# Optimization experiments

Hardware: AMD Instinct MI355X
Metric: run time of the kernel (lower is better)

The kernel has to match this reference:

```python
import jax, jax.numpy as jnp
import numpy as np
from jax import lax

POOL = 2  # pool_kernel

def _conv2d(x, w, b, stride=1):
    # x: [N,C,H,W], w: [O,I,kh,kw] (torch OIHW layout)
    y = lax.conv_general_dilated(
        x, w, window_strides=(stride, stride), padding='VALID',
        dimension_numbers=('NCHW', 'OIHW', 'NCHW'))
    return y + b[None, :, None, None]

def _maxpool(x, k):
    return lax.reduce_window(x, -jnp.inf, lax.max,
                             (1, 1, k, k), (1, 1, k, k), 'VALID')

def setup_inputs() -> dict:
    key = jax.random.key(0)
    ks = jax.random.split(key, 8)
    B, S, D = 8, 64, 128
    C = 32  # num_channels, depth=3 -> channels 1->32->64->64
    def kaiming(k, shape):
        fan_in = shape[1] * shape[2] * shape[3]
        return jax.random.normal(k, shape, jnp.float32) * np.float32(np.sqrt(2.0 / fan_in))
    return {
        'token_features': jax.random.normal(ks[0], (B, S, D), jnp.float32),
        'type_embedds': jax.random.normal(ks[1], (B, S, D), jnp.float32),
        'w0': kaiming(ks[2], (C, 1, 3, 3)),
        'b0': jnp.zeros((C,), jnp.float32),
        'w1': kaiming(ks[3], (2 * C, C, 3, 3)),
        'b1': jnp.zeros((2 * C,), jnp.float32),
        'w2': kaiming(ks[4], (2 * C, 2 * C, 3, 3)),
        'b2': jnp.zeros((2 * C,), jnp.float32),
    }

def reference(token_features, type_embedds, w0, b0, w1, b1, w2, b2):
    B, S, D = type_embedds.shape
    # Outter2dFusion: ger(gate, features) -> fused[b,s,i,j] = type[b,s,i]*token[b,s,j]
    fused = jnp.einsum('bsi,bsj->bsij', type_embedds, token_features)
    x = fused.reshape(B * S, 1, D, D)  # each token's d x d map as 1-channel image
    gelu = lambda t: jax.nn.gelu(t, approximate=False)  # torch GELU default (erf)
    x = _maxpool(gelu(_conv2d(x, w0, b0, stride=1)), POOL)
    x = _maxpool(gelu(_conv2d(x, w1, b1, stride=1)), POOL)
    x = _maxpool(gelu(_conv2d(x, w2, b2, stride=1)), POOL)
    # dropout is identity at inference
    return x.reshape(B, S, -1)
```

## Files before the change

### kernel.cpp

```cpp
#include <hip/hip_runtime.h>


typedef short short8 __attribute__((ext_vector_type(8)));
typedef float f32x4 __attribute__((ext_vector_type(4)));

#define OFF_TY   0
#define OFF_TK   512
#define OFF_HLO  1024
#define OFF_HHI  (1024 + 16128)
#define OFF_P0   (17152 + 8064)
#define OFF_P1   (25216 + 16896)
#define LDS_TOTAL (42112 + 1472*16)

__device__ __forceinline__ unsigned short f2bf(float f) {
    unsigned int u = __float_as_uint(f);
    u += 0x7fffu + ((u >> 16) & 1u);
    return (unsigned short)(u >> 16);
}

__device__ __forceinline__ float gelu_f(float x) {
    float ax = __builtin_fabsf(x);
    float E  = __builtin_amdgcn_exp2f(x * x * -0.72134752f);
    float k  = __builtin_amdgcn_rcpf(__builtin_fmaf(0.33267686f, ax, 1.0f));
    float s  = __builtin_fmaf(0.7478556f, k, -0.0958798f);
    s = __builtin_fmaf(s, k, 0.3480242f);
    s = s * k;
    float erfabs = __builtin_fmaf(-s, E, 1.0f);
    return __builtin_fmaf(0.5f * ax, erfabs, 0.5f * x);
}

__device__ __forceinline__ void produce(char* smem, const float* tys,
                                        float b0r, int c, int tid, int R0) {
    float t0 = tys[2*R0+0], t1 = tys[2*R0+1], t2 = tys[2*R0+2],
          t3 = tys[2*R0+3], t4 = tys[2*R0+4], t5 = tys[2*R0+5];
    int rest = tid >> 5;
    #pragma unroll
    for (int k = 0; k < 8; ++k, rest += 16) {
        if (rest < 126) {
            int roff = (rest >= 63) ? 1 : 0;
            int q = rest - (roff ? 63 : 0);
            float s0 = roff ? t2 : t0;
            float s1 = roff ? t3 : t1;
            float s2 = roff ? t4 : t2;
            float s3 = roff ? t5 : t3;
            uint2 lo = *(const uint2*)(smem + OFF_HLO + (c*126 + 2*q)*4);
            unsigned int hi = *(const unsigned int*)(smem + OFF_HHI + (c*126 + 2*q)*2);
            float h00 = __uint_as_float(lo.x << 16);
            float h10 = __uint_as_float(lo.x & 0xffff0000u);
            float h01 = __uint_as_float(lo.y << 16);
            float h11 = __uint_as_float(lo.y & 0xffff0000u);
            float h20 = __uint_as_float(hi << 16);
            float h21 = __uint_as_float(hi & 0xffff0000u);
            float e00 = __builtin_fmaf(s0,h00, __builtin_fmaf(s1,h10, __builtin_fmaf(s2,h20, b0r)));
            float e10 = __builtin_fmaf(s1,h00, __builtin_fmaf(s2,h10, __builtin_fmaf(s3,h20, b0r)));
            float e01 = __builtin_fmaf(s0,h01, __builtin_fmaf(s1,h11, __builtin_fmaf(s2,h21, b0r)));
            float e11 = __builtin_fmaf(s1,h01, __builtin_fmaf(s2,h11, __builtin_fmaf(s3,h21, b0r)));
            float m = gelu_f(fmaxf(fmaxf(e00, e01), fmaxf(e10, e11)));
            int slot = (R0 + roff) & 3;
            int unit = slot*264 + (q>>1)*8 + ((4*(q&1) + (c>>3)) ^ ((q>>1)&7));
            *(unsigned short*)(smem + OFF_P0 + unit*16 + (c&7)*2) = f2bf(m);
        }
    }
}

__launch_bounds__(512, 2)
__global__ void conv_pipeline(const float* __restrict__ token,
                              const float* __restrict__ type_,
                              const float* __restrict__ w0, const float* __restrict__ b0,
                              const float* __restrict__ w1, const float* __restrict__ b1,
                              const float* __restrict__ w2, const float* __restrict__ b2,
                              float* __restrict__ out) {
    extern __shared__ char smem[];
    float* tys = (float*)(smem + OFF_TY);
    float* tks = (float*)(smem + OFF_TK);

    const int tid = threadIdx.x;
    const int img = blockIdx.x;
    const int w   = tid >> 6;
    const int l   = tid & 63;
    const int l15 = l & 15;
    const int lc  = l >> 4;
    const int c0w = tid & 31;

    for (int i = tid; i < 128; i += 512) {
        tys[i] = type_[img*128 + i];
        tks[i] = token[img*128 + i];
    }

    const float b0r = b0[c0w];

    __syncthreads();

    {
        float w0r[9];
        #pragma unroll
        for (int i = 0; i < 9; ++i) w0r[i] = w0[c0w*9 + i];
        int x = tid >> 5;
        #pragma unroll
        for (int k = 0; k < 8; ++k, x += 16) {
            if (x < 126) {
                float t0 = tks[x], t1 = tks[x+1], t2 = tks[x+2];
                float h0 = __builtin_fmaf(w0r[0],t0, __builtin_fmaf(w0r[1],t1, w0r[2]*t2));
                float h1 = __builtin_fmaf(w0r[3],t0, __builtin_fmaf(w0r[4],t1, w0r[5]*t2));
                float h2 = __builtin_fmaf(w0r[6],t0, __builtin_fmaf(w0r[7],t1, w0r[8]*t2));
                unsigned int lov = (unsigned int)f2bf(h0) | ((unsigned int)f2bf(h1) << 16);
                *(unsigned int*)(smem + OFF_HLO + (c0w*126 + x)*4) = lov;
                *(unsigned short*)(smem + OFF_HHI + (c0w*126 + x)*2) = f2bf(h2);
            }
        }
    }

    short8 wf[18];
    float bias;
    const int ch = ((w & 3) * 16) + l15;
    if (w < 4) {
        bias = b1[ch];
        #pragma unroll
        for (int uv = 0; uv < 9; ++uv) {
            short8 f;
            #pragma unroll
            for (int j = 0; j < 8; ++j)
                f[j] = (short)f2bf(w1[(ch*32 + 8*lc + j)*9 + uv]);
            wf[uv] = f;
        }
    } else {
        bias = b2[ch];
        #pragma unroll
        for (int kh = 0; kh < 2; ++kh)
            #pragma unroll
            for (int uv = 0; uv < 9; ++uv) {
                short8 f;
                #pragma unroll
                for (int j = 0; j < 8; ++j)
                    f[j] = (short)f2bf(w2[(ch*64 + kh*32 + 8*lc + j)*9 + uv]);
                wf[kh*9 + uv] = f;
            }
    }

    __syncthreads();

    produce(smem, tys, b0r, c0w, tid, 0);
    produce(smem, tys, b0r, c0w, tid, 2);

    const size_t obase = (size_t)img * 12544;

    for (int i1 = 0; i1 < 30; ++i1) {
        __syncthreads();

        if (w < 4) {
            int rbase = (i1 % 6) * 30;
            int xr = ch >> 3;
            #pragma unroll
            for (int half = 0; half < 2; ++half) {
                f32x4 acc[4];
                #pragma unroll
                for (int i = 0; i < 4; ++i) acc[i] = (f32x4){0.f,0.f,0.f,0.f};
                #pragma unroll
                for (int pr = 0; pr < 4; ++pr) {
                    int sbase = ((2*i1 + pr) & 3) * 264;
                    #pragma unroll
                    for (int v = 0; v < 3; ++v) {
                        #pragma unroll
                        for (int mtl = 0; mtl < 2; ++mtl) {
                            int col = (2*half + mtl)*16 + l15 + v;
                            int unit = sbase + (col>>1)*8 + ((4*(col&1) + lc) ^ ((col>>1)&7));
                            short8 a = *(const short8*)(smem + OFF_P0 + unit*16);
                            if (pr <= 2)
                                acc[mtl*2+0] = __builtin_amdgcn_mfma_f32_16x16x32_bf16(
                                    a, wf[pr*3+v], acc[mtl*2+0], 0, 0, 0);
                            if (pr >= 1)
                                acc[mtl*2+1] = __builtin_amdgcn_mfma_f32_16x16x32_bf16(
                                    a, wf[(pr-1)*3+v], acc[mtl*2+1], 0, 0, 0);
                        }
                    }
                }
                #pragma unroll
                for (int mtl = 0; mtl < 2; ++mtl) {
                    int pcol = (2*half + mtl)*8 + lc*2;
                    if (pcol < 30) {
                        f32x4 A0 = acc[mtl*2+0], A1 = acc[mtl*2+1];
                        float p0 = fmaxf(fmaxf(A0[0], A0[1]), fmaxf(A1[0], A1[1]));
                        float p1 = fmaxf(fmaxf(A0[2], A0[3]), fmaxf(A1[2], A1[3]));
                        float m0 = gelu_f(p0 + bias);
                        float m1 = gelu_f(p1 + bias);
                        int u0 = (rbase + pcol)*8     + (xr ^ (pcol & 7));
                        int u1 = (rbase + pcol + 1)*8 + (xr ^ ((pcol+1) & 7));
                        *(unsigned short*)(smem + OFF_P1 + u0*16 + (ch&7)*2) = f2bf(m0);
                        *(unsigned short*)(smem + OFF_P1 + u1*16 + (ch&7)*2) = f2bf(m1);
                    }
                }
            }
        } else if (i1 >= 4 && (i1 & 1) == 0) {
            const int i2 = (i1 - 4) >> 1;
            f32x4 acc[4];
            #pragma unroll
            for (int i = 0; i < 4; ++i) acc[i] = (f32x4){0.f,0.f,0.f,0.f};
            #pragma unroll
            for (int pr = 0; pr < 4; ++pr) {
                int rb = ((2*i2 + pr) % 6) * 30;
                #pragma unroll
                for (int v = 0; v < 3; ++v) {
                    #pragma unroll
                    for (int mt = 0; mt < 2; ++mt) {
                        int col = mt*16 + l15 + v;
                        #pragma unroll
                        for (int kh = 0; kh < 2; ++kh) {
                            int unit = (rb + col)*8 + ((kh*4 + lc) ^ (col & 7));
                            short8 a = *(const short8*)(smem + OFF_P1 + unit*16);
                            if (pr <= 2)
                                acc[mt*2+0] = __builtin_amdgcn_mfma_f32_16x16x32_bf16(
                                    a, wf[kh*9 + pr*3+v], acc[mt*2+0], 0, 0, 0);
                            if (pr >= 1)
                                acc[mt*2+1] = __builtin_amdgcn_mfma_f32_16x16x32_bf16(
                                    a, wf[kh*9 + (pr-1)*3+v], acc[mt*2+1], 0, 0, 0);
                        }
                    }
                }
            }
            #pragma unroll
            for (int mt = 0; mt < 2; ++mt) {
                int pcol = mt*8 + lc*2;
                if (pcol < 14) {
                    f32x4 A0 = acc[mt*2+0], A1 = acc[mt*2+1];
                    float g00 = gelu_f(A0[0] + bias), g01 = gelu_f(A0[1] + bias);
                    float g02 = gelu_f(A0[2] + bias), g03 = gelu_f(A0[3] + bias);
                    float g10 = gelu_f(A1[0] + bias), g11 = gelu_f(A1[1] + bias);
                    float g12 = gelu_f(A1[2] + bias), g13 = gelu_f(A1[3] + bias);
                    float m0 = fmaxf(fmaxf(g00, g01), fmaxf(g10, g11));
                    float m1 = fmaxf(fmaxf(g02, g03), fmaxf(g12, g13));
                    float2 st; st.x = m0; st.y = m1;
                    *(float2*)(out + obase + ch*196 + i2*14 + pcol) = st;
                }
            }
        }

        __syncthreads();
        if (i1 < 29) produce(smem, tys, b0r, c0w, tid, 2*i1 + 4);
    }

    __syncthreads();
    if (w >= 4) {
        const int i2 = 13;
        f32x4 acc[4];
        #pragma unroll
        for (int i = 0; i < 4; ++i) acc[i] = (f32x4){0.f,0.f,0.f,0.f};
        #pragma unroll
        for (int pr = 0; pr < 4; ++pr) {
            int rb = ((2*i2 + pr) % 6) * 30;
            #pragma unroll
            for (int v = 0; v < 3; ++v) {
                #pragma unroll
                for (int mt = 0; mt < 2; ++mt) {
                    int col = mt*16 + l15 + v;
                    #pragma unroll
                    for (int kh = 0; kh < 2; ++kh) {
                        int unit = (rb + col)*8 + ((kh*4 + lc) ^ (col & 7));
                        short8 a = *(const short8*)(smem + OFF_P1 + unit*16);
                        if (pr <= 2)
                            acc[mt*2+0] = __builtin_amdgcn_mfma_f32_16x16x32_bf16(
                                a, wf[kh*9 + pr*3+v], acc[mt*2+0], 0, 0, 0);
                        if (pr >= 1)
                            acc[mt*2+1] = __builtin_amdgcn_mfma_f32_16x16x32_bf16(
                                a, wf[kh*9 + (pr-1)*3+v], acc[mt*2+1], 0, 0, 0);
                    }
                }
            }
        }
        #pragma unroll
        for (int mt = 0; mt < 2; ++mt) {
            int pcol = mt*8 + lc*2;
            if (pcol < 14) {
                f32x4 A0 = acc[mt*2+0], A1 = acc[mt*2+1];
                float g00 = gelu_f(A0[0] + bias), g01 = gelu_f(A0[1] + bias);
                float g02 = gelu_f(A0[2] + bias), g03 = gelu_f(A0[3] + bias);
                float g10 = gelu_f(A1[0] + bias), g11 = gelu_f(A1[1] + bias);
                float g12 = gelu_f(A1[2] + bias), g13 = gelu_f(A1[3] + bias);
                float m0 = fmaxf(fmaxf(g00, g01), fmaxf(g10, g11));
                float m1 = fmaxf(fmaxf(g02, g03), fmaxf(g12, g13));
                float2 st; st.x = m0; st.y = m1;
                *(float2*)(out + obase + ch*196 + i2*14 + pcol) = st;
            }
        }
    }
}

extern "C" void kernel_launch(void* const* d_in, const int* in_sizes, int n_in,
                              void* d_out, int out_size, void* d_ws, size_t ws_size,
                              hipStream_t stream) {
    const float* token = (const float*)d_in[0];
    const float* type_ = (const float*)d_in[1];
    const float* w0 = (const float*)d_in[2];
    const float* b0 = (const float*)d_in[3];
    const float* w1 = (const float*)d_in[4];
    const float* b1 = (const float*)d_in[5];
    const float* w2 = (const float*)d_in[6];
    const float* b2 = (const float*)d_in[7];
    float* out = (float*)d_out;

    hipLaunchKernelGGL(conv_pipeline, dim3(512), dim3(512), LDS_TOTAL, stream,
                       token, type_, w0, b0, w1, b1, w2, b2, out);
}
```

Measured before the change: 194.1 us.

## Compute conv0 with fp16 MFMA in bursts over a 16-slot pool0 ring

Replaces the scalar FMA conv0 producer with fp16 MFMA tiles. The separable row-factor products are stored as fp16 in a new LDS layout, and each burst of MFMAs produces eight pooled rows at once. The pool0 ring buffer grows from 4 to 16 slots, so conv0 runs only every fourth iteration, and one barrier per loop iteration is removed. In exchange, LDS use rises to about 124 KB, which may cut occupancy below 2 blocks per CU, and it adds fp16 rounding plus zero-padded MFMA work.

Measured after the change: 187.3 us. -3.5%, faster.

```diff
diff --git a/kernel.cpp b/kernel.cpp
--- a/kernel.cpp
+++ b/kernel.cpp
@@ -2,20 +2,28 @@
 
 
 typedef short short8 __attribute__((ext_vector_type(8)));
+typedef _Float16 half8 __attribute__((ext_vector_type(8)));
 typedef float f32x4 __attribute__((ext_vector_type(4)));
+typedef unsigned int uint4v __attribute__((ext_vector_type(4)));
 
 #define OFF_TY   0
-#define OFF_TK   512
-#define OFF_HLO  1024
-#define OFF_HHI  (1024 + 16128)
-#define OFF_P0   (17152 + 8064)
-#define OFF_P1   (25216 + 16896)
-#define LDS_TOTAL (42112 + 1472*16)
+#define OFF_H16  544
+#define OFF_P0   32800
+#define OFF_P1   100384
+#define OFF_TK   OFF_P0
+#define LDS_TOTAL 123936
 
 __device__ __forceinline__ unsigned short f2bf(float f) {
     unsigned int u = __float_as_uint(f);
     u += 0x7fffu + ((u >> 16) & 1u);
     return (unsigned short)(u >> 16);
+}
+
+__device__ __forceinline__ unsigned int pack2h(float a, float b) {
+    union { _Float16 h[2]; unsigned int u; } p;
+    p.h[0] = (_Float16)a;
+    p.h[1] = (_Float16)b;
+    return p.u;
 }
 
 __device__ __forceinline__ float gelu_f(float x) {
@@ -29,36 +37,49 @@
     return __builtin_fmaf(0.5f * ax, erfabs, 0.5f * x);
 }
 
-__device__ __forceinline__ void produce(char* smem, const float* tys,
-                                        float b0r, int c, int tid, int R0) {
-    float t0 = tys[2*R0+0], t1 = tys[2*R0+1], t2 = tys[2*R0+2],
-          t3 = tys[2*R0+3], t4 = tys[2*R0+4], t5 = tys[2*R0+5];
-    int rest = tid >> 5;
+__device__ __forceinline__ void conv0_burst(char* smem, const float* tys,
+                                            int w, int l15, int lc,
+                                            float b00, float b01, int pbase) {
+    const int y_base = 2 * pbase;
+    half8 afrag;
+    {
+        float a0 = tys[y_base + l15 + 0];
+        float a1 = tys[y_base + l15 + 1];
+        float a2 = tys[y_base + l15 + 2];
+        float a3 = tys[y_base + l15 + 3];
+        union { uint4v u; half8 h; } av;
+        av.u = (uint4v){ pack2h(a0, a1), pack2h(a2, a3), 0u, 0u };
+        afrag = av.h;
+    }
+    const f32x4 ci0 = (f32x4){b00, b00, b00, b00};
+    const f32x4 ci1 = (f32x4){b01, b01, b01, b01};
+    const int base = (w < 4) ? w * 12 : 48 + (w - 4) * 20;
+    const int cnt  = (w < 4) ? 12 : ((w == 7) ? 18 : 20);
+
     #pragma unroll
-    for (int k = 0; k < 8; ++k, rest += 16) {
-        if (rest < 126) {
-            int roff = (rest >= 63) ? 1 : 0;
-            int q = rest - (roff ? 63 : 0);
-            float s0 = roff ? t2 : t0;
-            float s1 = roff ? t3 : t1;
-            float s2 = roff ? t4 : t2;
-            float s3 = roff ? t5 : t3;
-            uint2 lo = *(const uint2*)(smem + OFF_HLO + (c*126 + 2*q)*4);
-            unsigned int hi = *(const unsigned int*)(smem + OFF_HHI + (c*126 + 2*q)*2);
-            float h00 = __uint_as_float(lo.x << 16);
-            float h10 = __uint_as_float(lo.x & 0xffff0000u);
-            float h01 = __uint_as_float(lo.y << 16);
-            float h11 = __uint_as_float(lo.y & 0xffff0000u);
-            float h20 = __uint_as_float(hi << 16);
-            float h21 = __uint_as_float(hi & 0xffff0000u);
-            float e00 = __builtin_fmaf(s0,h00, __builtin_fmaf(s1,h10, __builtin_fmaf(s2,h20, b0r)));
-            float e10 = __builtin_fmaf(s1,h00, __builtin_fmaf(s2,h10, __builtin_fmaf(s3,h20, b0r)));
-            float e01 = __builtin_fmaf(s0,h01, __builtin_fmaf(s1,h11, __builtin_fmaf(s2,h21, b0r)));
-            float e11 = __builtin_fmaf(s1,h01, __builtin_fmaf(s2,h11, __builtin_fmaf(s3,h21, b0r)));
-            float m = gelu_f(fmaxf(fmaxf(e00, e01), fmaxf(e10, e11)));
-            int slot = (R0 + roff) & 3;
-            int unit = slot*264 + (q>>1)*8 + ((4*(q&1) + (c>>3)) ^ ((q>>1)&7));
-            *(unsigned short*)(smem + OFF_P0 + unit*16 + (c&7)*2) = f2bf(m);
+    for (int j = 0; j < 20; ++j) {
+        if (j < cnt) {
+            const int uid = base + j;
+            const int q  = uid >> 1;
+            const int ct = uid & 1;
+            const char* hp = smem + OFF_H16 + ((2*q)*32 + ct*16 + l15) * 8;
+            uint2 hA = *(const uint2*)(hp);
+            uint2 hB = *(const uint2*)(hp + 256);
+            if (lc != 0) { hA.x = 0u; hA.y = 0u; hB.x = 0u; hB.y = 0u; }
+            union { uint4v u; half8 h; } ba, bb;
+            ba.u = (uint4v){hA.x, hA.y, 0u, 0u};
+            bb.u = (uint4v){hB.x, hB.y, 0u, 0u};
+            const f32x4 ci = ct ? ci1 : ci0;
+            f32x4 cA = __builtin_amdgcn_mfma_f32_16x16x32_f16(afrag, ba.h, ci, 0, 0, 0);
+            f32x4 cB = __builtin_amdgcn_mfma_f32_16x16x32_f16(afrag, bb.h, ci, 0, 0, 0);
+            float m0 = gelu_f(fmaxf(fmaxf(cA[0], cA[1]), fmaxf(cB[0], cB[1])));
+            float m1 = gelu_f(fmaxf(fmaxf(cA[2], cA[3]), fmaxf(cB[2], cB[3])));
+            const int c = ct * 16 + l15;
+            const int upos = (q >> 1) * 8 + ((4 * (q & 1) + (c >> 3)) ^ ((q >> 1) & 7));
+            const int p0 = pbase + 2 * lc;
+            const int s0 = p0 & 15, s1 = (p0 + 1) & 15;
+            *(unsigned short*)(smem + OFF_P0 + (s0 * 264 + upos) * 16 + (c & 7) * 2) = f2bf(m0);
+            *(unsigned short*)(smem + OFF_P0 + (s1 * 264 + upos) * 16 + (c & 7) * 2) = f2bf(m1);
         }
     }
 }
@@ -82,12 +103,13 @@
     const int lc  = l >> 4;
     const int c0w = tid & 31;
 
-    for (int i = tid; i < 128; i += 512) {
-        tys[i] = type_[img*128 + i];
-        tks[i] = token[img*128 + i];
-    }
-
-    const float b0r = b0[c0w];
+    for (int i = tid; i < 132; i += 512) {
+        tys[i] = (i < 128) ? type_[img*128 + i] : 0.f;
+        if (i < 128) tks[i] = token[img*128 + i];
+    }
+
+    const float b00 = b0[l15];
+    const float b01 = b0[l15 + 16];
 
     __syncthreads();
 
@@ -103,9 +125,8 @@
                 float h0 = __builtin_fmaf(w0r[0],t0, __builtin_fmaf(w0r[1],t1, w0r[2]*t2));
                 float h1 = __builtin_fmaf(w0r[3],t0, __builtin_fmaf(w0r[4],t1, w0r[5]*t2));
                 float h2 = __builtin_fmaf(w0r[6],t0, __builtin_fmaf(w0r[7],t1, w0r[8]*t2));
-                unsigned int lov = (unsigned int)f2bf(h0) | ((unsigned int)f2bf(h1) << 16);
-                *(unsigned int*)(smem + OFF_HLO + (c0w*126 + x)*4) = lov;
-                *(unsigned short*)(smem + OFF_HHI + (c0w*126 + x)*2) = f2bf(h2);
+                uint2 hv; hv.x = pack2h(h0, h1); hv.y = pack2h(h2, 0.f);
+                *(uint2*)(smem + OFF_H16 + (x*32 + c0w)*8) = hv;
             }
         }
     }
@@ -139,14 +160,12 @@
 
     __syncthreads();
 
-    produce(smem, tys, b0r, c0w, tid, 0);
-    produce(smem, tys, b0r, c0w, tid, 2);
+    conv0_burst(smem, tys, w, l15, lc, b00, b01, 0);
+    __syncthreads();
 
     const size_t obase = (size_t)img * 12544;
 
     for (int i1 = 0; i1 < 30; ++i1) {
-        __syncthreads();
-
         if (w < 4) {
             int rbase = (i1 % 6) * 30;
             int xr = ch >> 3;
@@ -157,7 +176,7 @@
                 for (int i = 0; i < 4; ++i) acc[i] = (f32x4){0.f,0.f,0.f,0.f};
                 #pragma unroll
                 for (int pr = 0; pr < 4; ++pr) {
-                    int sbase = ((2*i1 + pr) & 3) * 264;
+                    int sbase = ((2*i1 + pr) & 15) * 264;
                     #pragma unroll
                     for (int v = 0; v < 3; ++v) {
                         #pragma unroll
@@ -234,11 +253,11 @@
             }
         }
 
+        if ((i1 & 3) == 2) conv0_burst(smem, tys, w, l15, lc, b00, b01, 2*i1 + 4);
+
         __syncthreads();
-        if (i1 < 29) produce(smem, tys, b0r, c0w, tid, 2*i1 + 4);
-    }
-
-    __syncthreads();
+    }
+
     if (w >= 4) {
         const int i2 = 13;
         f32x4 acc[4];
```
